# Performance work log

Measured on AMD Instinct MI355X. Metric: run time of the kernel, lower is better.

The kernel has to match this reference:

```python
import jax, jax.numpy as jnp
import numpy as np

B, S, L, F = 32, 48, 64, 256


def setup_inputs() -> dict:
    key = jax.random.key(0)
    ks = jax.random.split(key, 7)
    return {
        "features": jax.random.normal(ks[0], (B, S, L, F), dtype=jnp.float32),
        "src_locs": jax.random.normal(ks[1], (B, L, 2), dtype=jnp.float32),
        "tar_locs": jax.random.normal(ks[2], (B, 2), dtype=jnp.float32),
        "W1": jax.random.normal(ks[3], (F, F), dtype=jnp.float32) * (1.0 / np.sqrt(F)),
        "b1": jax.random.normal(ks[4], (F,), dtype=jnp.float32) * 0.02,
        "W2": jax.random.normal(ks[5], (F, 1), dtype=jnp.float32) * (1.0 / np.sqrt(F)),
        "b2": jax.random.normal(ks[6], (1,), dtype=jnp.float32) * 0.02,
    }


def reference(features, src_locs, tar_locs, W1, b1, W2, b2):
    # features: (B, S, L, F); src_locs: (B, L, 2); tar_locs: (B, 2)
    # MLP score: Linear(F,F) + ReLU + Linear(F,1) + ReLU -> (B, S, L, 1)
    attn = jax.nn.relu(jnp.einsum('bslf,fg->bslg', features, W1) + b1)
    attn = jax.nn.relu(jnp.einsum('bslf,fo->bslo', attn, W2) + b2)  # (B,S,L,1)
    # inverse-distance weights over stations: (B, L)
    dists = jnp.sqrt(jnp.sum((src_locs - tar_locs[:, None, :]) ** 2, axis=-1))
    inv_dists = 1.0 / dists  # (B, L)
    # broadcast to (B, 1, L, 1), softmax over src_length axis (axis=2)
    attn_scores = jax.nn.softmax(attn * inv_dists[:, None, :, None], axis=2)
    # weighted sum over stations -> (B, S, F)
    return jnp.sum(features * attn_scores, axis=2)
```

## Files before the change

kernel.cpp:

```cpp
#include <hip/hip_runtime.h>
#include <hip/hip_fp16.h>
#include <math.h>

typedef _Float16 half8 __attribute__((ext_vector_type(8)));
typedef float floatx4 __attribute__((ext_vector_type(4)));

#define BB 32
#define SS 48
#define LL 64
#define FF 256

#define WAVE_BARRIER() do {                                          \
    asm volatile("s_waitcnt lgkmcnt(0)" ::: "memory");               \
    __builtin_amdgcn_s_barrier();                                    \
    asm volatile("" ::: "memory");                                   \
} while (0)

#define ISSUE_FENCE() asm volatile("" ::: "memory")

__global__ __launch_bounds__(256) void prep_w(const float* __restrict__ W1,
                                              _Float16* __restrict__ whi,
                                              _Float16* __restrict__ wlo) {
    int idx = blockIdx.x * 256 + threadIdx.x;
    int j    = idx & 7;
    int lane = (idx >> 3) & 63;
    int nt   = (idx >> 9) & 15;
    int kt   = idx >> 13;
    int k = kt * 32 + ((lane >> 4) & 3) * 8 + j;
    int n = nt * 16 + (lane & 15);
    float x = W1[k * FF + n];
    _Float16 hi = (_Float16)x;
    _Float16 lo = (_Float16)(x - (float)hi);
    whi[idx] = hi;
    wlo[idx] = lo;
}

__global__ __launch_bounds__(512, 4) void ida_mfma(
    const float* __restrict__ features,
    const float* __restrict__ src_locs,
    const float* __restrict__ tar_locs,
    const _Float16* __restrict__ whi,
    const _Float16* __restrict__ wlo,
    const float* __restrict__ b1,
    const float* __restrict__ W2,
    const float* __restrict__ b2,
    float* __restrict__ out)
{
    __shared__ __align__(16) unsigned char smem[32768];
    _Float16* Ahi = (_Float16*)smem;
    _Float16* Alo = (_Float16*)(smem + 16384);
    float* SP  = (float*)smem;
    float* red = SP + LL * 8;

    const int t    = threadIdx.x;
    const int w    = t >> 6;
    const int lane = t & 63;
    const int quad = lane >> 4;
    const int l16  = lane & 15;
    const int bs   = blockIdx.x;
    const int b    = bs / SS;

    const float* Xg = features + (size_t)bs * (LL * FF);

    float sx = src_locs[(b * LL + lane) * 2 + 0];
    float sy = src_locs[(b * LL + lane) * 2 + 1];
    float tx = tar_locs[b * 2 + 0];
    float ty = tar_locs[b * 2 + 1];
    float b2v = b2[0];
    ISSUE_FENCE();

    float4 a0raw[4];
    #pragma unroll
    for (int it = 0; it < 2; ++it) {
        int g   = it * 8 + w;
        int row = (g >> 2) * 16 + l16;
        int kc  = (g & 3) * 32 + quad * 8;
        const float4* p = (const float4*)(Xg + row * FF + kc);
        a0raw[2 * it + 0] = p[0];
        a0raw[2 * it + 1] = p[1];
    }
    ISSUE_FENCE();

    half8 bh[2], bl[2], nbh[2], nbl[2];
    #pragma unroll
    for (int ntl = 0; ntl < 2; ++ntl) {
        size_t off = ((size_t)(0 * 16 + (w * 2 + ntl)) * 64 + lane) * 8;
        bh[ntl] = *((const half8*)(whi + off));
        bl[ntl] = *((const half8*)(wlo + off));
    }
    ISSUE_FENCE();

    float4 a1raw[4];
    #pragma unroll
    for (int it = 0; it < 2; ++it) {
        int g   = it * 8 + w;
        int row = (g >> 2) * 16 + l16;
        int kc  = (g & 3) * 32 + quad * 8;
        const float4* p = (const float4*)(Xg + row * FF + 128 + kc);
        a1raw[2 * it + 0] = p[0];
        a1raw[2 * it + 1] = p[1];
    }
    ISSUE_FENCE();

    #pragma unroll
    for (int it = 0; it < 2; ++it) {
        int g = it * 8 + w;
        float4 x0 = a0raw[2 * it + 0], x1 = a0raw[2 * it + 1];
        float xs[8] = {x0.x, x0.y, x0.z, x0.w, x1.x, x1.y, x1.z, x1.w};
        half8 hi, lo;
        #pragma unroll
        for (int j = 0; j < 8; ++j) {
            _Float16 h = (_Float16)xs[j];
            hi[j] = h;
            lo[j] = (_Float16)(xs[j] - (float)h);
        }
        *((half8*)&Ahi[(g * 64 + lane) * 8]) = hi;
        *((half8*)&Alo[(g * 64 + lane) * 8]) = lo;
    }

    WAVE_BARRIER();

    floatx4 acc[4][2] = {};

    float b1v[2], w2v[2];
    #pragma unroll
    for (int ntl = 0; ntl < 2; ++ntl) {
        int n = (w * 2 + ntl) * 16 + l16;
        b1v[ntl] = b1[n];
        w2v[ntl] = W2[n];
    }

#define COMPUTE_HALF(h)                                                          \
    _Pragma("unroll")                                                            \
    for (int ktl = 0; ktl < 4; ++ktl) {                                          \
        if (ktl < 3) {                                                           \
            _Pragma("unroll")                                                    \
            for (int ntl = 0; ntl < 2; ++ntl) {                                  \
                size_t off = ((size_t)(((h) * 4 + ktl + 1) * 16 + (w * 2 + ntl)) * 64 + lane) * 8; \
                nbh[ntl] = *((const half8*)(whi + off));                         \
                nbl[ntl] = *((const half8*)(wlo + off));                         \
            }                                                                    \
        }                                                                        \
        _Pragma("unroll")                                                        \
        for (int mt = 0; mt < 4; ++mt) {                                         \
            half8 ahi = *((half8*)&Ahi[((mt * 4 + ktl) * 64 + lane) * 8]);       \
            half8 alo = *((half8*)&Alo[((mt * 4 + ktl) * 64 + lane) * 8]);       \
            _Pragma("unroll")                                                    \
            for (int ntl = 0; ntl < 2; ++ntl) {                                  \
                acc[mt][ntl] = __builtin_amdgcn_mfma_f32_16x16x32_f16(ahi, bh[ntl], acc[mt][ntl], 0, 0, 0); \
                acc[mt][ntl] = __builtin_amdgcn_mfma_f32_16x16x32_f16(ahi, bl[ntl], acc[mt][ntl], 0, 0, 0); \
                acc[mt][ntl] = __builtin_amdgcn_mfma_f32_16x16x32_f16(alo, bh[ntl], acc[mt][ntl], 0, 0, 0); \
            }                                                                    \
        }                                                                        \
        if (ktl < 3) {                                                           \
            bh[0] = nbh[0]; bh[1] = nbh[1];                                      \
            bl[0] = nbl[0]; bl[1] = nbl[1];                                      \
        }                                                                        \
    }

    COMPUTE_HALF(0)

    #pragma unroll
    for (int ntl = 0; ntl < 2; ++ntl) {
        size_t off = ((size_t)(4 * 16 + (w * 2 + ntl)) * 64 + lane) * 8;
        bh[ntl] = *((const half8*)(whi + off));
        bl[ntl] = *((const half8*)(wlo + off));
    }

    WAVE_BARRIER();

    #pragma unroll
    for (int it = 0; it < 2; ++it) {
        int g = it * 8 + w;
        float4 x0 = a1raw[2 * it + 0], x1 = a1raw[2 * it + 1];
        float xs[8] = {x0.x, x0.y, x0.z, x0.w, x1.x, x1.y, x1.z, x1.w};
        half8 hi, lo;
        #pragma unroll
        for (int j = 0; j < 8; ++j) {
            _Float16 h = (_Float16)xs[j];
            hi[j] = h;
            lo[j] = (_Float16)(xs[j] - (float)h);
        }
        *((half8*)&Ahi[(g * 64 + lane) * 8]) = hi;
        *((half8*)&Alo[(g * 64 + lane) * 8]) = lo;
    }

    WAVE_BARRIER();

    COMPUTE_HALF(1)
#undef COMPUTE_HALF

    float4 xraw[8];
    {
        const float4* Xg4 = (const float4*)Xg;
        #pragma unroll
        for (int lr = 0; lr < 8; ++lr)
            xraw[lr] = Xg4[(w * 8 + lr) * 64 + lane];
    }
    ISSUE_FENCE();

    WAVE_BARRIER();

    #pragma unroll
    for (int mt = 0; mt < 4; ++mt) {
        #pragma unroll
        for (int r = 0; r < 4; ++r) {
            float p = 0.f;
            #pragma unroll
            for (int ntl = 0; ntl < 2; ++ntl) {
                float h = fmaxf(acc[mt][ntl][r] + b1v[ntl], 0.f);
                p = fmaf(h, w2v[ntl], p);
            }
            p += __shfl_xor(p, 1);
            p += __shfl_xor(p, 2);
            p += __shfl_xor(p, 4);
            p += __shfl_xor(p, 8);
            if (l16 == 0) SP[(mt * 16 + quad * 4 + r) * 8 + w] = p;
        }
    }

    WAVE_BARRIER();

    float s = SP[8 * lane + 0] + SP[8 * lane + 1] + SP[8 * lane + 2] + SP[8 * lane + 3]
            + SP[8 * lane + 4] + SP[8 * lane + 5] + SP[8 * lane + 6] + SP[8 * lane + 7] + b2v;
    float score = fmaxf(s, 0.f);
    float dxv = sx - tx, dyv = sy - ty;
    float inv_d = 1.0f / sqrtf(dxv * dxv + dyv * dyv);
    float logit = score * inv_d;
    float m = logit;
    #pragma unroll
    for (int o = 32; o > 0; o >>= 1) m = fmaxf(m, __shfl_xor(m, o));
    float e = __expf(logit - m);
    float se = e;
    #pragma unroll
    for (int o = 32; o > 0; o >>= 1) se += __shfl_xor(se, o);
    float wgt = e / se;

    {
        floatx4 o4 = {0.f, 0.f, 0.f, 0.f};
        #pragma unroll
        for (int lr = 0; lr < 8; ++lr) {
            float wl = __shfl(wgt, w * 8 + lr);
            o4[0] = fmaf(xraw[lr].x, wl, o4[0]);
            o4[1] = fmaf(xraw[lr].y, wl, o4[1]);
            o4[2] = fmaf(xraw[lr].z, wl, o4[2]);
            o4[3] = fmaf(xraw[lr].w, wl, o4[3]);
        }
        *((floatx4*)&red[w * FF + lane * 4]) = o4;
    }

    WAVE_BARRIER();

    if (t < FF) {
        float o = red[0 * FF + t] + red[1 * FF + t] + red[2 * FF + t] + red[3 * FF + t]
                + red[4 * FF + t] + red[5 * FF + t] + red[6 * FF + t] + red[7 * FF + t];
        out[(size_t)bs * FF + t] = o;
    }
}

extern "C" void kernel_launch(void* const* d_in, const int* in_sizes, int n_in,
                              void* d_out, int out_size, void* d_ws, size_t ws_size,
                              hipStream_t stream) {
    const float* features = (const float*)d_in[0];
    const float* src_locs = (const float*)d_in[1];
    const float* tar_locs = (const float*)d_in[2];
    const float* W1       = (const float*)d_in[3];
    const float* b1       = (const float*)d_in[4];
    const float* W2       = (const float*)d_in[5];
    const float* b2       = (const float*)d_in[6];
    float* out = (float*)d_out;

    _Float16* whi = (_Float16*)d_ws;
    _Float16* wlo = whi + FF * FF;

    prep_w<<<dim3(FF * FF / 256), dim3(256), 0, stream>>>(W1, whi, wlo);
    ida_mfma<<<dim3(BB * SS), dim3(512), 0, stream>>>(
        features, src_locs, tar_locs, whi, wlo, b1, W2, b2, out);
}
```

Baseline: 183.1 us.

## Drop feature low-part MFMA split and reuse fp16 LDS tile for weighted sum

The first GEMM now converts features to fp16 only, with no hi/lo split. This cuts the MFMA count per tile from three to two while keeping the split of W1. The whole 64x256 tile is loaded and staged in LDS in one pass instead of two halves. The final weighted sum reads the fp16 features back from LDS rather than reloading fp32 features from global memory. This removes global traffic and MFMA work, but accepts fp16 rounding in both the scores and the output, and the larger LDS footprint may reduce blocks per CU.

```diff
diff --git a/kernel.cpp b/kernel.cpp
--- a/kernel.cpp
+++ b/kernel.cpp
@@ -3,6 +3,7 @@
 #include <math.h>
 
 typedef _Float16 half8 __attribute__((ext_vector_type(8)));
+typedef _Float16 half4_t __attribute__((ext_vector_type(4)));
 typedef float floatx4 __attribute__((ext_vector_type(4)));
 
 #define BB 32
@@ -46,11 +47,9 @@
     const float* __restrict__ b2,
     float* __restrict__ out)
 {
-    __shared__ __align__(16) unsigned char smem[32768];
-    _Float16* Ahi = (_Float16*)smem;
-    _Float16* Alo = (_Float16*)(smem + 16384);
-    float* SP  = (float*)smem;
-    float* red = SP + LL * 8;
+    __shared__ _Float16 Ahi[16384];
+    __shared__ float SP[LL * 8];
+    __shared__ float red[8 * FF];
 
     const int t    = threadIdx.x;
     const int w    = t >> 6;
@@ -67,17 +66,24 @@
     float tx = tar_locs[b * 2 + 0];
     float ty = tar_locs[b * 2 + 1];
     float b2v = b2[0];
+    float b1v[2], w2v[2];
+    #pragma unroll
+    for (int ntl = 0; ntl < 2; ++ntl) {
+        int n = (w * 2 + ntl) * 16 + l16;
+        b1v[ntl] = b1[n];
+        w2v[ntl] = W2[n];
+    }
     ISSUE_FENCE();
 
-    float4 a0raw[4];
-    #pragma unroll
-    for (int it = 0; it < 2; ++it) {
-        int g   = it * 8 + w;
-        int row = (g >> 2) * 16 + l16;
-        int kc  = (g & 3) * 32 + quad * 8;
-        const float4* p = (const float4*)(Xg + row * FF + kc);
-        a0raw[2 * it + 0] = p[0];
-        a0raw[2 * it + 1] = p[1];
+    float4 araw[8];
+    #pragma unroll
+    for (int it = 0; it < 4; ++it) {
+        int G   = it * 8 + w;
+        int row = (G >> 3) * 16 + l16;
+        int cb  = (G & 7) * 32 + quad * 8;
+        const float4* p = (const float4*)(Xg + row * FF + cb);
+        araw[2 * it + 0] = p[0];
+        araw[2 * it + 1] = p[1];
     }
     ISSUE_FENCE();
 
@@ -90,116 +96,45 @@
     }
     ISSUE_FENCE();
 
-    float4 a1raw[4];
-    #pragma unroll
-    for (int it = 0; it < 2; ++it) {
-        int g   = it * 8 + w;
-        int row = (g >> 2) * 16 + l16;
-        int kc  = (g & 3) * 32 + quad * 8;
-        const float4* p = (const float4*)(Xg + row * FF + 128 + kc);
-        a1raw[2 * it + 0] = p[0];
-        a1raw[2 * it + 1] = p[1];
-    }
-    ISSUE_FENCE();
-
-    #pragma unroll
-    for (int it = 0; it < 2; ++it) {
-        int g = it * 8 + w;
-        float4 x0 = a0raw[2 * it + 0], x1 = a0raw[2 * it + 1];
+    #pragma unroll
+    for (int it = 0; it < 4; ++it) {
+        int G = it * 8 + w;
+        float4 x0 = araw[2 * it + 0], x1 = araw[2 * it + 1];
         float xs[8] = {x0.x, x0.y, x0.z, x0.w, x1.x, x1.y, x1.z, x1.w};
-        half8 hi, lo;
-        #pragma unroll
-        for (int j = 0; j < 8; ++j) {
-            _Float16 h = (_Float16)xs[j];
-            hi[j] = h;
-            lo[j] = (_Float16)(xs[j] - (float)h);
-        }
-        *((half8*)&Ahi[(g * 64 + lane) * 8]) = hi;
-        *((half8*)&Alo[(g * 64 + lane) * 8]) = lo;
+        half8 hi;
+        #pragma unroll
+        for (int j = 0; j < 8; ++j) hi[j] = (_Float16)xs[j];
+        *((half8*)&Ahi[(G * 64 + lane) * 8]) = hi;
     }
 
     WAVE_BARRIER();
 
     floatx4 acc[4][2] = {};
 
-    float b1v[2], w2v[2];
-    #pragma unroll
-    for (int ntl = 0; ntl < 2; ++ntl) {
-        int n = (w * 2 + ntl) * 16 + l16;
-        b1v[ntl] = b1[n];
-        w2v[ntl] = W2[n];
-    }
-
-#define COMPUTE_HALF(h)                                                          \
-    _Pragma("unroll")                                                            \
-    for (int ktl = 0; ktl < 4; ++ktl) {                                          \
-        if (ktl < 3) {                                                           \
-            _Pragma("unroll")                                                    \
-            for (int ntl = 0; ntl < 2; ++ntl) {                                  \
-                size_t off = ((size_t)(((h) * 4 + ktl + 1) * 16 + (w * 2 + ntl)) * 64 + lane) * 8; \
-                nbh[ntl] = *((const half8*)(whi + off));                         \
-                nbl[ntl] = *((const half8*)(wlo + off));                         \
-            }                                                                    \
-        }                                                                        \
-        _Pragma("unroll")                                                        \
-        for (int mt = 0; mt < 4; ++mt) {                                         \
-            half8 ahi = *((half8*)&Ahi[((mt * 4 + ktl) * 64 + lane) * 8]);       \
-            half8 alo = *((half8*)&Alo[((mt * 4 + ktl) * 64 + lane) * 8]);       \
-            _Pragma("unroll")                                                    \
-            for (int ntl = 0; ntl < 2; ++ntl) {                                  \
-                acc[mt][ntl] = __builtin_amdgcn_mfma_f32_16x16x32_f16(ahi, bh[ntl], acc[mt][ntl], 0, 0, 0); \
-                acc[mt][ntl] = __builtin_amdgcn_mfma_f32_16x16x32_f16(ahi, bl[ntl], acc[mt][ntl], 0, 0, 0); \
-                acc[mt][ntl] = __builtin_amdgcn_mfma_f32_16x16x32_f16(alo, bh[ntl], acc[mt][ntl], 0, 0, 0); \
-            }                                                                    \
-        }                                                                        \
-        if (ktl < 3) {                                                           \
-            bh[0] = nbh[0]; bh[1] = nbh[1];                                      \
-            bl[0] = nbl[0]; bl[1] = nbl[1];                                      \
-        }                                                                        \
-    }
-
-    COMPUTE_HALF(0)
-
-    #pragma unroll
-    for (int ntl = 0; ntl < 2; ++ntl) {
-        size_t off = ((size_t)(4 * 16 + (w * 2 + ntl)) * 64 + lane) * 8;
-        bh[ntl] = *((const half8*)(whi + off));
-        bl[ntl] = *((const half8*)(wlo + off));
-    }
-
-    WAVE_BARRIER();
-
-    #pragma unroll
-    for (int it = 0; it < 2; ++it) {
-        int g = it * 8 + w;
-        float4 x0 = a1raw[2 * it + 0], x1 = a1raw[2 * it + 1];
-        float xs[8] = {x0.x, x0.y, x0.z, x0.w, x1.x, x1.y, x1.z, x1.w};
-        half8 hi, lo;
-        #pragma unroll
-        for (int j = 0; j < 8; ++j) {
-            _Float16 h = (_Float16)xs[j];
-            hi[j] = h;
-            lo[j] = (_Float16)(xs[j] - (float)h);
-        }
-        *((half8*)&Ahi[(g * 64 + lane) * 8]) = hi;
-        *((half8*)&Alo[(g * 64 + lane) * 8]) = lo;
-    }
-
-    WAVE_BARRIER();
-
-    COMPUTE_HALF(1)
-#undef COMPUTE_HALF
-
-    float4 xraw[8];
-    {
-        const float4* Xg4 = (const float4*)Xg;
-        #pragma unroll
-        for (int lr = 0; lr < 8; ++lr)
-            xraw[lr] = Xg4[(w * 8 + lr) * 64 + lane];
-    }
-    ISSUE_FENCE();
-
-    WAVE_BARRIER();
+    #pragma unroll
+    for (int kt = 0; kt < 8; ++kt) {
+        if (kt < 7) {
+            #pragma unroll
+            for (int ntl = 0; ntl < 2; ++ntl) {
+                size_t off = ((size_t)((kt + 1) * 16 + (w * 2 + ntl)) * 64 + lane) * 8;
+                nbh[ntl] = *((const half8*)(whi + off));
+                nbl[ntl] = *((const half8*)(wlo + off));
+            }
+        }
+        #pragma unroll
+        for (int mt = 0; mt < 4; ++mt) {
+            half8 ahi = *((half8*)&Ahi[((mt * 8 + kt) * 64 + lane) * 8]);
+            #pragma unroll
+            for (int ntl = 0; ntl < 2; ++ntl) {
+                acc[mt][ntl] = __builtin_amdgcn_mfma_f32_16x16x32_f16(ahi, bh[ntl], acc[mt][ntl], 0, 0, 0);
+                acc[mt][ntl] = __builtin_amdgcn_mfma_f32_16x16x32_f16(ahi, bl[ntl], acc[mt][ntl], 0, 0, 0);
+            }
+        }
+        if (kt < 7) {
+            bh[0] = nbh[0]; bh[1] = nbh[1];
+            bl[0] = nbl[0]; bl[1] = nbl[1];
+        }
+    }
 
     #pragma unroll
     for (int mt = 0; mt < 4; ++mt) {
@@ -240,11 +175,15 @@
         floatx4 o4 = {0.f, 0.f, 0.f, 0.f};
         #pragma unroll
         for (int lr = 0; lr < 8; ++lr) {
-            float wl = __shfl(wgt, w * 8 + lr);
-            o4[0] = fmaf(xraw[lr].x, wl, o4[0]);
-            o4[1] = fmaf(xraw[lr].y, wl, o4[1]);
-            o4[2] = fmaf(xraw[lr].z, wl, o4[2]);
-            o4[3] = fmaf(xraw[lr].w, wl, o4[3]);
+            int r  = w * 8 + lr;
+            float wl = __shfl(wgt, r);
+            int G2 = (r >> 4) * 8 + (lane >> 3);
+            int ei = (G2 * 64 + ((lane >> 1) & 3) * 16 + (r & 15)) * 8 + (lane & 1) * 4;
+            half4_t hv = *((const half4_t*)&Ahi[ei]);
+            o4[0] = fmaf((float)hv[0], wl, o4[0]);
+            o4[1] = fmaf((float)hv[1], wl, o4[1]);
+            o4[2] = fmaf((float)hv[2], wl, o4[2]);
+            o4[3] = fmaf((float)hv[3], wl, o4[3]);
         }
         *((floatx4*)&red[w * FF + lane * 4]) = o4;
     }
```

New measurement: 182.7 us. About the same (-0.2%).
